# Kernel optimization log

Measured on AMD Instinct MI355X. Metric: run time of the kernel, lower is better.

The kernel has to match this reference:

```python
import jax, jax.numpy as jnp
import numpy as np

GROUP_SIZE = 128  # QuantizationConfig default


def setup_inputs() -> dict:
    key = jax.random.key(0)
    k0, k1, k2, k3 = jax.random.split(key, 4)
    B, IN, OUT = 32, 4096, 16384
    NG = IN // GROUP_SIZE  # 32 groups
    x = jax.random.normal(k0, (B, IN), dtype=jnp.float16)
    # int8 symmetric-quantized weights in [-127, 127]
    qweight = jax.random.randint(k1, (OUT, IN), -127, 128, dtype=jnp.int8)
    # per-(out_channel, group) fp16 scales; small positive values as produced by absmax/127
    scales = (jax.random.uniform(k2, (OUT, NG), dtype=jnp.float16) * jnp.float16(0.01)
              + jnp.float16(1e-3))
    bias = jax.random.normal(k3, (OUT,), dtype=jnp.float16) * jnp.float16(0.01)
    return {"x": x, "qweight": qweight, "scales": scales, "bias": bias}


def reference(x, qweight, scales, bias):
    # QuantizedLinear._forward_grouped, sym=True, in_features % group_size == 0 path.
    OUT, IN = qweight.shape
    NG = IN // GROUP_SIZE
    # dequantize: [OUT, NG, G] * [OUT, NG, 1] -> [OUT, IN], all in fp16
    w_deq = (qweight.astype(jnp.float16).reshape(OUT, NG, GROUP_SIZE)
             * scales[:, :, None]).reshape(OUT, IN)
    # F.linear(x, w_deq) = x @ w_deq.T, then + bias
    out = jnp.dot(x, w_deq.T) + bias
    return out
```

## Files before the change

### kernel.cpp

```cpp
#include <hip/hip_runtime.h>

typedef __attribute__((ext_vector_type(8))) short short8;
typedef __attribute__((ext_vector_type(4))) float f32x4;
typedef __attribute__((ext_vector_type(4))) int   i32x4;

#define IN_F   4096
#define OUT_F  16384
#define NG     32
#define BK     128
#define NCHUNK 16

static __device__ __forceinline__ short f2bf(float f) {
    union { float f; unsigned u; } c; c.f = f;
    unsigned u = c.u;
    u += 0x7FFF + ((u >> 16) & 1);
    return (short)(u >> 16);
}

static __device__ __forceinline__ short i2bf(int v) {
    union { float f; unsigned u; } c; c.f = (float)v;
    return (short)(c.u >> 16);
}

__global__ __launch_bounds__(256)
void xconv_kernel(const float* __restrict__ x, unsigned short* __restrict__ xT) {
    const int g   = blockIdx.x * 256 + threadIdx.x;
    const int t   = g >> 7;
    const int rem = g & 127;
    const int h   = rem >> 6;
    const int ln  = rem & 63;
    const int l15 = ln >> 2;
    const int l4  = ln & 3;
    const float* src = x + (size_t)(16 * h + l15) * IN_F + t * 32 + l4 * 8;
    f32x4 a = *(const f32x4*)src;
    f32x4 b = *(const f32x4*)(src + 4);
    short8 o;
#pragma unroll
    for (int j = 0; j < 4; ++j) { o[j] = f2bf(a[j]); o[j + 4] = f2bf(b[j]); }
    *(short8*)(xT + (size_t)g * 8) = o;
}

__global__ __launch_bounds__(512, 4)
void qlin_kernel(const unsigned short* __restrict__ xT,
                 const int*   __restrict__ qw,
                 const float* __restrict__ scales,
                 const float* __restrict__ bias,
                 float*       __restrict__ out)
{
    __shared__ int   lqw[2][2][32][BK];
    __shared__ float red[8][64][4];

    const int tid  = threadIdx.x;
    const int wv   = tid >> 6;
    const int lane = tid & 63;
    const int l15  = lane & 15;
    const int l4   = lane >> 4;
    const int wk   = wv >> 2;
    const int wm   = (wv >> 1) & 1;
    const int wn   = wv & 1;
    const int col0 = blockIdx.x * 32;

    auto STAGE = [&](int c, int b) {
        const int widx = wv & 3;
        const size_t kbase = (size_t)wk * 2048 + (size_t)c * BK;
#pragma unroll
        for (int i = 0; i < 4; ++i) {
            const int p   = widx * 4 + i;
            const int row = 2 * p + (lane >> 5);
            const int byt = ((lane & 31) * 16) ^ ((row & 7) << 4);
            const char* src = (const char*)(qw + (size_t)(col0 + row) * IN_F + kbase) + byt;
            __builtin_amdgcn_global_load_lds(
                (const __attribute__((address_space(1))) unsigned int*)src,
                (__attribute__((address_space(3))) unsigned int*)&lqw[wk][b][2 * p][0],
                16, 0, 0);
        }
    };

    const int rowB = 16 * wn + l15;
    const int swzB = (rowB & 7) << 4;
    const char* lrow_base0 = (const char*)&lqw[wk][0][rowB][0];
    const char* lrow_base1 = (const char*)&lqw[wk][1][rowB][0];
    const unsigned short* xgrp = xT + (size_t)(l15 * 4 + l4) * 8 + (size_t)wm * 512;

    f32x4 acc = {0.f, 0.f, 0.f, 0.f};

    auto COMPUTE = [&](int c, int b) {
        const char* lrow = b ? lrow_base1 : lrow_base0;
        f32x4 ag = {0.f, 0.f, 0.f, 0.f};
#pragma unroll
        for (int s = 0; s < 4; ++s) {
            const int t = wk * 64 + c * 4 + s;
            short8 a = *(const short8*)(xgrp + (size_t)t * 1024);
            const int byte0 = (s * 128 + l4 * 32) ^ swzB;
            i32x4 q0 = *(const i32x4*)(lrow + byte0);
            i32x4 q1 = *(const i32x4*)(lrow + (byte0 ^ 16));
            short8 bfr;
#pragma unroll
            for (int j = 0; j < 4; ++j) { bfr[j] = i2bf(q0[j]); bfr[j + 4] = i2bf(q1[j]); }
            ag = __builtin_amdgcn_mfma_f32_16x16x32_bf16(a, bfr, ag, 0, 0, 0);
        }
        const float sc = scales[(size_t)(col0 + rowB) * NG + wk * 16 + c];
#pragma unroll
        for (int r = 0; r < 4; ++r) acc[r] += sc * ag[r];
    };

    STAGE(0, 0);
    __syncthreads();
    int cur = 0;
    for (int c = 0; c < NCHUNK - 1; ++c) {
        STAGE(c + 1, cur ^ 1);
        COMPUTE(c, cur);
        __syncthreads();
        cur ^= 1;
    }
    COMPUTE(NCHUNK - 1, cur);

#pragma unroll
    for (int r = 0; r < 4; ++r) red[wv][lane][r] = acc[r];
    __syncthreads();
    if (wv < 4) {
        const int col = col0 + rowB;
        const float bv = bias[col];
#pragma unroll
        for (int r = 0; r < 4; ++r) {
            const float v = red[wv][lane][r] + red[wv + 4][lane][r] + bv;
            out[(size_t)(16 * wm + l4 * 4 + r) * OUT_F + col] = v;
        }
    }
}

extern "C" void kernel_launch(void* const* d_in, const int* in_sizes, int n_in,
                              void* d_out, int out_size, void* d_ws, size_t ws_size,
                              hipStream_t stream) {
    const float* x      = (const float*)d_in[0];
    const int*   qw     = (const int*)d_in[1];
    const float* scales = (const float*)d_in[2];
    const float* bias   = (const float*)d_in[3];
    float*       out    = (float*)d_out;
    unsigned short* xT  = (unsigned short*)d_ws;

    hipLaunchKernelGGL(xconv_kernel, dim3(64), dim3(256), 0, stream, x, xT);
    hipLaunchKernelGGL(qlin_kernel, dim3(OUT_F / 32), dim3(512), 0, stream,
                       xT, qw, scales, bias, out);
}
```

Measured before the change: 57.45 us.

## Triple-buffer half-group weight chunks with explicit vmcnt waits and register-prefetched activations

Halves the K chunk to 64 and replaces the double-buffered loop with a three-slot LDS ring. Raw s_barrier plus s_waitcnt vmcnt keeps two weight stages in flight across each barrier. Activation fragments are prefetched into registers two chunks ahead, and per-group scales are loaded once up front. The reduction buffer now reuses the weight LDS, which lowers shared-memory use and may allow more blocks per CU. The cost is twice as many barriers and hand-written wait counts that must exactly match the number of outstanding loads.

After: 52.61 us. -8.4%, faster.

```diff
diff --git a/kernel.cpp b/kernel.cpp
--- a/kernel.cpp
+++ b/kernel.cpp
@@ -7,8 +7,8 @@
 #define IN_F   4096
 #define OUT_F  16384
 #define NG     32
-#define BK     128
-#define NCHUNK 16
+#define BK     64
+#define NCH    32
 
 static __device__ __forceinline__ short f2bf(float f) {
     union { float f; unsigned u; } c; c.f = f;
@@ -47,8 +47,7 @@
                  const float* __restrict__ bias,
                  float*       __restrict__ out)
 {
-    __shared__ int   lqw[2][2][32][BK];
-    __shared__ float red[8][64][4];
+    __shared__ int lqw[2][3][32][BK];
 
     const int tid  = threadIdx.x;
     const int wv   = tid >> 6;
@@ -58,74 +57,96 @@
     const int wk   = wv >> 2;
     const int wm   = (wv >> 1) & 1;
     const int wn   = wv & 1;
+    const int widx = wv & 3;
     const int col0 = blockIdx.x * 32;
 
-    auto STAGE = [&](int c, int b) {
-        const int widx = wv & 3;
+    const int rowB = 16 * wn + l15;
+    const int swzB = (rowB & 7) << 4;
+
+    auto STAGE = [&](int c, int sl) {
         const size_t kbase = (size_t)wk * 2048 + (size_t)c * BK;
 #pragma unroll
-        for (int i = 0; i < 4; ++i) {
-            const int p   = widx * 4 + i;
-            const int row = 2 * p + (lane >> 5);
-            const int byt = ((lane & 31) * 16) ^ ((row & 7) << 4);
+        for (int i = 0; i < 2; ++i) {
+            const int p   = widx * 2 + i;
+            const int row = 4 * p + (lane >> 4);
+            const int byt = ((lane & 15) * 16) ^ ((row & 7) << 4);
             const char* src = (const char*)(qw + (size_t)(col0 + row) * IN_F + kbase) + byt;
             __builtin_amdgcn_global_load_lds(
                 (const __attribute__((address_space(1))) unsigned int*)src,
-                (__attribute__((address_space(3))) unsigned int*)&lqw[wk][b][2 * p][0],
+                (__attribute__((address_space(3))) unsigned int*)&lqw[wk][sl][4 * p][0],
                 16, 0, 0);
         }
     };
 
-    const int rowB = 16 * wn + l15;
-    const int swzB = (rowB & 7) << 4;
-    const char* lrow_base0 = (const char*)&lqw[wk][0][rowB][0];
-    const char* lrow_base1 = (const char*)&lqw[wk][1][rowB][0];
     const unsigned short* xgrp = xT + (size_t)(l15 * 4 + l4) * 8 + (size_t)wm * 512;
+    short8 xa[2][2];
+    auto XLOAD = [&](int c, int par) {
+        const int t = wk * 64 + c * 2;
+        xa[par][0] = *(const short8*)(xgrp + (size_t)t * 1024);
+        xa[par][1] = *(const short8*)(xgrp + (size_t)(t + 1) * 1024);
+    };
+
+    const float* scr = scales + (size_t)(col0 + rowB) * NG + wk * 16;
+    f32x4 sc4[4];
+#pragma unroll
+    for (int j = 0; j < 4; ++j) sc4[j] = *(const f32x4*)(scr + 4 * j);
 
     f32x4 acc = {0.f, 0.f, 0.f, 0.f};
 
-    auto COMPUTE = [&](int c, int b) {
-        const char* lrow = b ? lrow_base1 : lrow_base0;
+    auto COMPUTE = [&](int c, int sl, int par, float sc) {
+        const char* lrow = (const char*)&lqw[wk][sl][rowB][0];
         f32x4 ag = {0.f, 0.f, 0.f, 0.f};
 #pragma unroll
-        for (int s = 0; s < 4; ++s) {
-            const int t = wk * 64 + c * 4 + s;
-            short8 a = *(const short8*)(xgrp + (size_t)t * 1024);
+        for (int s = 0; s < 2; ++s) {
             const int byte0 = (s * 128 + l4 * 32) ^ swzB;
             i32x4 q0 = *(const i32x4*)(lrow + byte0);
             i32x4 q1 = *(const i32x4*)(lrow + (byte0 ^ 16));
             short8 bfr;
 #pragma unroll
             for (int j = 0; j < 4; ++j) { bfr[j] = i2bf(q0[j]); bfr[j + 4] = i2bf(q1[j]); }
-            ag = __builtin_amdgcn_mfma_f32_16x16x32_bf16(a, bfr, ag, 0, 0, 0);
+            ag = __builtin_amdgcn_mfma_f32_16x16x32_bf16(xa[par][s], bfr, ag, 0, 0, 0);
         }
-        const float sc = scales[(size_t)(col0 + rowB) * NG + wk * 16 + c];
 #pragma unroll
         for (int r = 0; r < 4; ++r) acc[r] += sc * ag[r];
     };
 
+    XLOAD(0, 0);
+    XLOAD(1, 1);
+    asm volatile("" ::: "memory");
     STAGE(0, 0);
-    __syncthreads();
-    int cur = 0;
-    for (int c = 0; c < NCHUNK - 1; ++c) {
-        STAGE(c + 1, cur ^ 1);
-        COMPUTE(c, cur);
-        __syncthreads();
-        cur ^= 1;
-    }
-    COMPUTE(NCHUNK - 1, cur);
+    STAGE(1, 1);
+    asm volatile("s_waitcnt vmcnt(2)" ::: "memory");
+    __builtin_amdgcn_s_barrier();
+    __builtin_amdgcn_sched_barrier(0);
 
 #pragma unroll
-    for (int r = 0; r < 4; ++r) red[wv][lane][r] = acc[r];
+    for (int i = 0; i <= 29; ++i) {
+        COMPUTE(i, i % 3, i & 1, sc4[(i >> 3)][(i >> 1) & 3]);
+        XLOAD(i + 2, i & 1);
+        asm volatile("" ::: "memory");
+        STAGE(i + 2, (i + 2) % 3);
+        asm volatile("s_waitcnt vmcnt(4)" ::: "memory");
+        __builtin_amdgcn_s_barrier();
+        __builtin_amdgcn_sched_barrier(0);
+    }
+    COMPUTE(30, 0, 0, sc4[3][3]);
+    asm volatile("s_waitcnt vmcnt(0)" ::: "memory");
+    __builtin_amdgcn_s_barrier();
+    __builtin_amdgcn_sched_barrier(0);
+    COMPUTE(31, 1, 1, sc4[3][3]);
+
+    __syncthreads();
+    float* red = (float*)&lqw[0][0][0][0];
+    *(f32x4*)&red[(size_t)(wv * 64 + lane) * 4] = acc;
     __syncthreads();
     if (wv < 4) {
         const int col = col0 + rowB;
         const float bv = bias[col];
+        f32x4 lo = *(const f32x4*)&red[(size_t)(wv * 64 + lane) * 4];
+        f32x4 hi = *(const f32x4*)&red[(size_t)((wv + 4) * 64 + lane) * 4];
 #pragma unroll
-        for (int r = 0; r < 4; ++r) {
-            const float v = red[wv][lane][r] + red[wv + 4][lane][r] + bv;
-            out[(size_t)(16 * wm + l4 * 4 + r) * OUT_F + col] = v;
-        }
+        for (int r = 0; r < 4; ++r)
+            out[(size_t)(16 * wm + l4 * 4 + r) * OUT_F + col] = lo[r] + hi[r] + bv;
     }
 }
 
```
